# Performance work log

Hardware: AMD Instinct MI355X
Metric: run time of the kernel (lower is better)

## Reference

```python
import jax, jax.numpy as jnp
import numpy as np

B, N, D, K = 8, 4096, 128, 1024


def setup_inputs() -> dict:
    key = jax.random.key(0)
    kx, kp = jax.random.split(key)
    x = jax.random.normal(kx, (B, N, D), dtype=jnp.float32)
    # matches nn.Parameter(...).uniform_(-0.1, 0.1)
    prototypes = jax.random.uniform(kp, (K, D), dtype=jnp.float32, minval=-0.1, maxval=0.1)
    return {"x": x, "prototypes": prototypes, "hard": 1}


def reference(x, prototypes, hard):
    x_sq = jnp.sum(x * x, axis=-1, keepdims=True)            # [B,N,1]
    p_sq = jnp.sum(prototypes * prototypes, axis=-1)         # [K]
    xp = jnp.einsum('bnd,kd->bnk', x, prototypes)            # [B,N,K]
    scores = -(x_sq + p_sq[None, None, :] - 2.0 * xp)        # [B,N,K]
    if bool(hard):
        idx = jnp.argmax(scores, axis=-1)                    # [B,N]
        matched = prototypes[idx]                            # [B,N,D]
    else:
        w = jax.nn.softmax(scores, axis=-1)                  # [B,N,K]
        matched = jnp.einsum('bnk,kd->bnd', w, prototypes)   # [B,N,D]
    return (matched, scores)
```

## Files before the change

### kernel.cpp

```cpp
#include <hip/hip_runtime.h>

typedef short short8 __attribute__((ext_vector_type(8)));
typedef float f32x4  __attribute__((ext_vector_type(4)));

constexpr int M_TOT  = 8 * 4096;
constexpr int K_PROT = 1024;
constexpr int D_DIM  = 128;

constexpr size_t WS_PSQ_OFF = (size_t)M_TOT * 4;
constexpr size_t WS_PF_OFF  = WS_PSQ_OFF + (size_t)K_PROT * 4;

__device__ inline unsigned short bf16_hi(float f) {
  unsigned u = __builtin_bit_cast(unsigned, f);
  unsigned r = u + 0x7FFFu + ((u >> 16) & 1u);
  return (unsigned short)(r >> 16);
}
__device__ inline float bf16_tof(unsigned short h) {
  return __builtin_bit_cast(float, (unsigned)h << 16);
}

__device__ inline void barrier_lds() {
  asm volatile("s_waitcnt lgkmcnt(0)\n\ts_barrier" ::: "memory");
}

__global__ __launch_bounds__(256) void norms_kernel(
    const float* __restrict__ x, const float* __restrict__ p,
    float* __restrict__ xsq, float* __restrict__ psq) {
  int group = blockIdx.x * (blockDim.x >> 5) + (threadIdx.x >> 5);
  int lane  = threadIdx.x & 31;
  if (group >= M_TOT + K_PROT) return;
  const float* row = (group < M_TOT) ? (x + (size_t)group * D_DIM)
                                     : (p + (size_t)(group - M_TOT) * D_DIM);
  float4 v = reinterpret_cast<const float4*>(row)[lane];
  float s = v.x * v.x + v.y * v.y + v.z * v.z + v.w * v.w;
  #pragma unroll
  for (int off = 16; off > 0; off >>= 1) s += __shfl_down(s, off, 32);
  if (lane == 0) {
    if (group < M_TOT) xsq[group] = s;
    else psq[group - M_TOT] = s;
  }
}

__global__ __launch_bounds__(256) void pfrag_kernel(
    const float* __restrict__ p, short* __restrict__ pf) {
  int g    = blockIdx.x * 256 + threadIdx.x;
  int lane = g & 63;
  int s    = (g >> 6) & 7;
  int ng   = g >> 9;
  int part = s >> 2, ks = s & 3;
  int proto = ng * 16 + (lane & 15);
  int k0    = ks * 32 + (lane >> 4) * 8;
  const float4* pr = (const float4*)(p + (size_t)proto * D_DIM + k0);
  float4 a = pr[0], b = pr[1];
  float e[8] = {a.x, a.y, a.z, a.w, b.x, b.y, b.z, b.w};
  short8 frag;
  #pragma unroll
  for (int j = 0; j < 8; ++j) {
    unsigned short h = bf16_hi(e[j]);
    if (part) h = bf16_hi(e[j] - bf16_tof(h));
    frag[j] = (short)h;
  }
  *(short8*)(pf + (size_t)g * 8) = frag;
}

__global__ __launch_bounds__(256, 2) void proto_mfma(
    const float* __restrict__ x, const float* __restrict__ p,
    const short* __restrict__ pf, const float* __restrict__ xsq,
    const float* __restrict__ psq,
    float* __restrict__ matched, float* __restrict__ scores) {
  __shared__ short xlds[32 * 64 * 8];
  __shared__ float sbuf[64][132];
  __shared__ float sv[4][64];
  __shared__ int   si[4][64];
  __shared__ int   fidx[64];

  const int tid = threadIdx.x;
  const int w   = tid >> 6;
  const int l   = tid & 63;
  const int m0  = blockIdx.x * 64;

  #pragma unroll
  for (int i = 0; i < 8; ++i) {
    int piece = i * 256 + tid;
    int lane = piece & 63;
    int s = piece >> 6;
    int ks = s & 3, nt = (s >> 2) & 3, part = s >> 4;
    int pix = m0 + nt * 16 + (lane & 15);
    int k0  = ks * 32 + (lane >> 4) * 8;
    const float4* xr = (const float4*)(x + (size_t)pix * D_DIM + k0);
    float4 a = xr[0], b = xr[1];
    float e[8] = {a.x, a.y, a.z, a.w, b.x, b.y, b.z, b.w};
    short8 frag;
    #pragma unroll
    for (int j = 0; j < 8; ++j) {
      unsigned short h = bf16_hi(e[j]);
      if (part) h = bf16_hi(e[j] - bf16_tof(h));
      frag[j] = (short)h;
    }
    *(short8*)(xlds + (size_t)piece * 8) = frag;
  }
  __syncthreads();

  float xs[4];
  #pragma unroll
  for (int nt = 0; nt < 4; ++nt) xs[nt] = xsq[m0 + nt * 16 + (l & 15)];

  float best[4]; int bidx[4];
  #pragma unroll
  for (int nt = 0; nt < 4; ++nt) { best[nt] = -3.4e38f; bidx[nt] = 0; }

  for (int chunk = 0; chunk < 4; ++chunk) {
    f32x4 acc[4][4];
    #pragma unroll
    for (int mt = 0; mt < 4; ++mt)
      #pragma unroll
      for (int nt = 0; nt < 4; ++nt) acc[mt][nt] = (f32x4){0.f, 0.f, 0.f, 0.f};

    const int pgbase = chunk * 16 + w * 4;

    #pragma unroll
    for (int ks = 0; ks < 4; ++ks) {
      short8 pah[4], pal[4], bh[4], bl[4];
      #pragma unroll
      for (int mt = 0; mt < 4; ++mt) {
        pah[mt] = *(const short8*)(pf + ((size_t)((pgbase + mt) * 8 + ks) * 64 + l) * 8);
        pal[mt] = *(const short8*)(pf + ((size_t)((pgbase + mt) * 8 + 4 + ks) * 64 + l) * 8);
      }
      #pragma unroll
      for (int nt = 0; nt < 4; ++nt) {
        bh[nt] = *(const short8*)(xlds + (size_t)(((nt * 4 + ks) * 64) + l) * 8);
        bl[nt] = *(const short8*)(xlds + (size_t)(((16 + nt * 4 + ks) * 64) + l) * 8);
      }
      #pragma unroll
      for (int mt = 0; mt < 4; ++mt)
        #pragma unroll
        for (int nt = 0; nt < 4; ++nt)
          acc[mt][nt] = __builtin_amdgcn_mfma_f32_16x16x32_bf16(pah[mt], bh[nt], acc[mt][nt], 0, 0, 0);
      #pragma unroll
      for (int mt = 0; mt < 4; ++mt)
        #pragma unroll
        for (int nt = 0; nt < 4; ++nt)
          acc[mt][nt] = __builtin_amdgcn_mfma_f32_16x16x32_bf16(pah[mt], bl[nt], acc[mt][nt], 0, 0, 0);
      #pragma unroll
      for (int mt = 0; mt < 4; ++mt)
        #pragma unroll
        for (int nt = 0; nt < 4; ++nt)
          acc[mt][nt] = __builtin_amdgcn_mfma_f32_16x16x32_bf16(pal[mt], bh[nt], acc[mt][nt], 0, 0, 0);
    }

    #pragma unroll
    for (int mt = 0; mt < 4; ++mt) {
      int pbase = chunk * 256 + w * 64 + mt * 16 + (l >> 4) * 4;
      float psa[4];
      *(float4*)psa = *(const float4*)(psq + pbase);
      #pragma unroll
      for (int nt = 0; nt < 4; ++nt) {
        f32x4 o;
        {
          #pragma clang fp contract(off)
          #pragma unroll
          for (int r = 0; r < 4; ++r) {
            float t = (xs[nt] + psa[r]) - 2.0f * acc[mt][nt][r];
            o[r] = -t;
            if (o[r] > best[nt]) { best[nt] = o[r]; bidx[nt] = pbase + r; }
          }
        }
        acc[mt][nt] = o;
      }
    }

    #pragma unroll
    for (int h = 0; h < 2; ++h) {
      if ((w >> 1) == h) {
        const int colbase = (w & 1) * 64 + (l >> 4) * 4;
        #pragma unroll
        for (int mt = 0; mt < 4; ++mt)
          #pragma unroll
          for (int nt = 0; nt < 4; ++nt)
            *(f32x4*)&sbuf[nt * 16 + (l & 15)][colbase + mt * 16] = acc[mt][nt];
      }
      barrier_lds();
      const int gbase = chunk * 256 + h * 128;
      #pragma unroll
      for (int ps = 0; ps < 8; ++ps) {
        int idx = ps * 256 + tid;
        int row = idx >> 5;
        int f4  = idx & 31;
        f32x4 v = *(const f32x4*)&sbuf[row][f4 * 4];
        *((f32x4*)(scores + (size_t)(m0 + row) * K_PROT + gbase + f4 * 4)) = v;
      }
      barrier_lds();
    }
  }

  #pragma unroll
  for (int nt = 0; nt < 4; ++nt) {
    #pragma unroll
    for (int m = 16; m <= 32; m <<= 1) {
      float ov = __shfl_xor(best[nt], m);
      int   oi = __shfl_xor(bidx[nt], m);
      if (ov > best[nt] || (ov == best[nt] && oi < bidx[nt])) {
        best[nt] = ov; bidx[nt] = oi;
      }
    }
  }
  if (l < 16) {
    #pragma unroll
    for (int nt = 0; nt < 4; ++nt) {
      sv[w][nt * 16 + l] = best[nt];
      si[w][nt * 16 + l] = bidx[nt];
    }
  }
  __syncthreads();
  if (tid < 64) {
    float v = sv[0][tid]; int bi = si[0][tid];
    #pragma unroll
    for (int e = 1; e < 4; ++e) {
      float vv = sv[e][tid]; int ii = si[e][tid];
      if (vv > v || (vv == v && ii < bi)) { v = vv; bi = ii; }
    }
    fidx[tid] = bi;
  }
  __syncthreads();

  for (int q = tid; q < 64 * 32; q += 256) {
    int pix = q >> 5, f4 = q & 31;
    float4 v = ((const float4*)(p + (size_t)fidx[pix] * D_DIM))[f4];
    *((f32x4*)(matched + (size_t)(m0 + pix) * D_DIM) + f4) = *(f32x4*)&v;
  }
}

extern "C" void kernel_launch(void* const* d_in, const int* in_sizes, int n_in,
                              void* d_out, int out_size, void* d_ws, size_t ws_size,
                              hipStream_t stream) {
  const float* x = (const float*)d_in[0];
  const float* p = (const float*)d_in[1];

  float* matched = (float*)d_out;
  float* scores  = (float*)d_out + (size_t)M_TOT * D_DIM;

  float* xsq = (float*)d_ws;
  float* psq = (float*)((char*)d_ws + WS_PSQ_OFF);
  short* pf  = (short*)((char*)d_ws + WS_PF_OFF);

  {
    int rows = M_TOT + K_PROT;
    int blocks = (rows + 7) / 8;
    norms_kernel<<<blocks, 256, 0, stream>>>(x, p, xsq, psq);
  }
  pfrag_kernel<<<128, 256, 0, stream>>>(p, pf);
  proto_mfma<<<M_TOT / 64, 256, 0, stream>>>(x, p, pf, xsq, psq, matched, scores);
}
```

Baseline: 184.7 us.

## Use per-wave swizzled LDS score staging, prefetch next-chunk fragments, merge prep kernels

Replaces the block-wide shared score buffer, which needed two barriers per half-chunk, with a per-wave XOR-swizzled LDS tile, so each wave writes out its own scores without block barriers. Prefetches the first-k-slice prototype fragments and the psq values for the next chunk while the stores drain. Merges the norms and fragment-prep kernels into one launch. LDS use rises to 32KB for score staging, which may reduce occupancy, and the prefetch raises register pressure.

```diff
diff --git a/kernel.cpp b/kernel.cpp
--- a/kernel.cpp
+++ b/kernel.cpp
@@ -9,6 +9,9 @@
 
 constexpr size_t WS_PSQ_OFF = (size_t)M_TOT * 4;
 constexpr size_t WS_PF_OFF  = WS_PSQ_OFF + (size_t)K_PROT * 4;
+
+constexpr int NORM_BLOCKS  = (M_TOT + K_PROT) / 8;
+constexpr int PFRAG_BLOCKS = 32768 / 256;
 
 __device__ inline unsigned short bf16_hi(float f) {
   unsigned u = __builtin_bit_cast(unsigned, f);
@@ -19,48 +22,45 @@
   return __builtin_bit_cast(float, (unsigned)h << 16);
 }
 
-__device__ inline void barrier_lds() {
-  asm volatile("s_waitcnt lgkmcnt(0)\n\ts_barrier" ::: "memory");
-}
-
-__global__ __launch_bounds__(256) void norms_kernel(
+__global__ __launch_bounds__(256) void prep_kernel(
     const float* __restrict__ x, const float* __restrict__ p,
-    float* __restrict__ xsq, float* __restrict__ psq) {
-  int group = blockIdx.x * (blockDim.x >> 5) + (threadIdx.x >> 5);
-  int lane  = threadIdx.x & 31;
-  if (group >= M_TOT + K_PROT) return;
-  const float* row = (group < M_TOT) ? (x + (size_t)group * D_DIM)
-                                     : (p + (size_t)(group - M_TOT) * D_DIM);
-  float4 v = reinterpret_cast<const float4*>(row)[lane];
-  float s = v.x * v.x + v.y * v.y + v.z * v.z + v.w * v.w;
-  #pragma unroll
-  for (int off = 16; off > 0; off >>= 1) s += __shfl_down(s, off, 32);
-  if (lane == 0) {
-    if (group < M_TOT) xsq[group] = s;
-    else psq[group - M_TOT] = s;
-  }
-}
-
-__global__ __launch_bounds__(256) void pfrag_kernel(
-    const float* __restrict__ p, short* __restrict__ pf) {
-  int g    = blockIdx.x * 256 + threadIdx.x;
-  int lane = g & 63;
-  int s    = (g >> 6) & 7;
-  int ng   = g >> 9;
-  int part = s >> 2, ks = s & 3;
-  int proto = ng * 16 + (lane & 15);
-  int k0    = ks * 32 + (lane >> 4) * 8;
-  const float4* pr = (const float4*)(p + (size_t)proto * D_DIM + k0);
-  float4 a = pr[0], b = pr[1];
-  float e[8] = {a.x, a.y, a.z, a.w, b.x, b.y, b.z, b.w};
-  short8 frag;
-  #pragma unroll
-  for (int j = 0; j < 8; ++j) {
-    unsigned short h = bf16_hi(e[j]);
-    if (part) h = bf16_hi(e[j] - bf16_tof(h));
-    frag[j] = (short)h;
-  }
-  *(short8*)(pf + (size_t)g * 8) = frag;
+    float* __restrict__ xsq, float* __restrict__ psq, short* __restrict__ pf) {
+  const int bx  = blockIdx.x;
+  const int tid = threadIdx.x;
+  if (bx < NORM_BLOCKS) {
+    int group = bx * 8 + (tid >> 5);
+    int lane  = tid & 31;
+    if (group >= M_TOT + K_PROT) return;
+    const float* row = (group < M_TOT) ? (x + (size_t)group * D_DIM)
+                                       : (p + (size_t)(group - M_TOT) * D_DIM);
+    float4 v = reinterpret_cast<const float4*>(row)[lane];
+    float s = v.x * v.x + v.y * v.y + v.z * v.z + v.w * v.w;
+    #pragma unroll
+    for (int off = 16; off > 0; off >>= 1) s += __shfl_down(s, off, 32);
+    if (lane == 0) {
+      if (group < M_TOT) xsq[group] = s;
+      else psq[group - M_TOT] = s;
+    }
+  } else {
+    int g    = (bx - NORM_BLOCKS) * 256 + tid;
+    int lane = g & 63;
+    int s    = (g >> 6) & 7;
+    int ng   = g >> 9;
+    int part = s >> 2, ks = s & 3;
+    int proto = ng * 16 + (lane & 15);
+    int k0    = ks * 32 + (lane >> 4) * 8;
+    const float4* pr = (const float4*)(p + (size_t)proto * D_DIM + k0);
+    float4 a = pr[0], b = pr[1];
+    float e[8] = {a.x, a.y, a.z, a.w, b.x, b.y, b.z, b.w};
+    short8 frag;
+    #pragma unroll
+    for (int j = 0; j < 8; ++j) {
+      unsigned short h = bf16_hi(e[j]);
+      if (part) h = bf16_hi(e[j] - bf16_tof(h));
+      frag[j] = (short)h;
+    }
+    *(short8*)(pf + (size_t)g * 8) = frag;
+  }
 }
 
 __global__ __launch_bounds__(256, 2) void proto_mfma(
@@ -69,24 +69,24 @@
     const float* __restrict__ psq,
     float* __restrict__ matched, float* __restrict__ scores) {
   __shared__ short xlds[32 * 64 * 8];
-  __shared__ float sbuf[64][132];
-  __shared__ float sv[4][64];
-  __shared__ int   si[4][64];
+  __shared__ float sw[4][2048];
+  __shared__ float svv[4][64];
+  __shared__ int   sii[4][64];
   __shared__ int   fidx[64];
 
-  const int tid = threadIdx.x;
-  const int w   = tid >> 6;
-  const int l   = tid & 63;
-  const int m0  = blockIdx.x * 64;
+  const int tid  = threadIdx.x;
+  const int w    = tid >> 6;
+  const int l    = tid & 63;
+  const int m0   = blockIdx.x * 64;
+  const int csub = (l >> 4) << 2;
 
   #pragma unroll
   for (int i = 0; i < 8; ++i) {
     int piece = i * 256 + tid;
-    int lane = piece & 63;
     int s = piece >> 6;
     int ks = s & 3, nt = (s >> 2) & 3, part = s >> 4;
-    int pix = m0 + nt * 16 + (lane & 15);
-    int k0  = ks * 32 + (lane >> 4) * 8;
+    int pix = m0 + nt * 16 + (l & 15);
+    int k0  = ks * 32 + (l >> 4) * 8;
     const float4* xr = (const float4*)(x + (size_t)pix * D_DIM + k0);
     float4 a = xr[0], b = xr[1];
     float e[8] = {a.x, a.y, a.z, a.w, b.x, b.y, b.z, b.w};
@@ -109,6 +109,18 @@
   #pragma unroll
   for (int nt = 0; nt < 4; ++nt) { best[nt] = -3.4e38f; bidx[nt] = 0; }
 
+  short8 ppah[4], ppal[4];
+  f32x4  cpsq[4];
+  {
+    const int pg0 = w * 4;
+    #pragma unroll
+    for (int mt = 0; mt < 4; ++mt) {
+      ppah[mt] = *(const short8*)(pf + ((size_t)((pg0 + mt) * 8 + 0) * 64 + l) * 8);
+      ppal[mt] = *(const short8*)(pf + ((size_t)((pg0 + mt) * 8 + 4) * 64 + l) * 8);
+      cpsq[mt] = *(const f32x4*)(psq + w * 64 + mt * 16 + csub);
+    }
+  }
+
   for (int chunk = 0; chunk < 4; ++chunk) {
     f32x4 acc[4][4];
     #pragma unroll
@@ -121,10 +133,15 @@
     #pragma unroll
     for (int ks = 0; ks < 4; ++ks) {
       short8 pah[4], pal[4], bh[4], bl[4];
-      #pragma unroll
-      for (int mt = 0; mt < 4; ++mt) {
-        pah[mt] = *(const short8*)(pf + ((size_t)((pgbase + mt) * 8 + ks) * 64 + l) * 8);
-        pal[mt] = *(const short8*)(pf + ((size_t)((pgbase + mt) * 8 + 4 + ks) * 64 + l) * 8);
+      if (ks == 0) {
+        #pragma unroll
+        for (int mt = 0; mt < 4; ++mt) { pah[mt] = ppah[mt]; pal[mt] = ppal[mt]; }
+      } else {
+        #pragma unroll
+        for (int mt = 0; mt < 4; ++mt) {
+          pah[mt] = *(const short8*)(pf + ((size_t)((pgbase + mt) * 8 + ks) * 64 + l) * 8);
+          pal[mt] = *(const short8*)(pf + ((size_t)((pgbase + mt) * 8 + 4 + ks) * 64 + l) * 8);
+        }
       }
       #pragma unroll
       for (int nt = 0; nt < 4; ++nt) {
@@ -150,9 +167,8 @@
 
     #pragma unroll
     for (int mt = 0; mt < 4; ++mt) {
-      int pbase = chunk * 256 + w * 64 + mt * 16 + (l >> 4) * 4;
-      float psa[4];
-      *(float4*)psa = *(const float4*)(psq + pbase);
+      int pbase = chunk * 256 + w * 64 + mt * 16 + csub;
+      float psa[4] = {cpsq[mt][0], cpsq[mt][1], cpsq[mt][2], cpsq[mt][3]};
       #pragma unroll
       for (int nt = 0; nt < 4; ++nt) {
         f32x4 o;
@@ -169,27 +185,38 @@
       }
     }
 
-    #pragma unroll
-    for (int h = 0; h < 2; ++h) {
-      if ((w >> 1) == h) {
-        const int colbase = (w & 1) * 64 + (l >> 4) * 4;
-        #pragma unroll
-        for (int mt = 0; mt < 4; ++mt)
-          #pragma unroll
-          for (int nt = 0; nt < 4; ++nt)
-            *(f32x4*)&sbuf[nt * 16 + (l & 15)][colbase + mt * 16] = acc[mt][nt];
-      }
-      barrier_lds();
-      const int gbase = chunk * 256 + h * 128;
+    if (chunk < 3) {
+      const int npg = pgbase + 16;
+      #pragma unroll
+      for (int mt = 0; mt < 4; ++mt) {
+        ppah[mt] = *(const short8*)(pf + ((size_t)((npg + mt) * 8 + 0) * 64 + l) * 8);
+        ppal[mt] = *(const short8*)(pf + ((size_t)((npg + mt) * 8 + 4) * 64 + l) * 8);
+        cpsq[mt] = *(const f32x4*)(psq + (chunk + 1) * 256 + w * 64 + mt * 16 + csub);
+      }
+    }
+
+    #pragma unroll
+    for (int mp = 0; mp < 2; ++mp) {
+      #pragma unroll
+      for (int mt2 = 0; mt2 < 2; ++mt2) {
+        int mt = mp * 2 + mt2;
+        #pragma unroll
+        for (int nt = 0; nt < 4; ++nt) {
+          int row = nt * 16 + (l & 15);
+          int col = mt2 * 16 + csub;
+          int idx = (row << 5) + (col ^ ((row & 7) << 2));
+          *(f32x4*)&sw[w][idx] = acc[mt][nt];
+        }
+      }
+      const int drow = l >> 3;
+      const int dcol = (l & 7) << 2;
       #pragma unroll
       for (int ps = 0; ps < 8; ++ps) {
-        int idx = ps * 256 + tid;
-        int row = idx >> 5;
-        int f4  = idx & 31;
-        f32x4 v = *(const f32x4*)&sbuf[row][f4 * 4];
-        *((f32x4*)(scores + (size_t)(m0 + row) * K_PROT + gbase + f4 * 4)) = v;
-      }
-      barrier_lds();
+        int row = (ps << 3) + drow;
+        int idx = (row << 5) + (dcol ^ (drow << 2));
+        f32x4 v = *(const f32x4*)&sw[w][idx];
+        *((f32x4*)(scores + (size_t)(m0 + row) * K_PROT + chunk * 256 + (w << 6) + (mp << 5)) + (l & 7)) = v;
+      }
     }
   }
 
@@ -207,16 +234,16 @@
   if (l < 16) {
     #pragma unroll
     for (int nt = 0; nt < 4; ++nt) {
-      sv[w][nt * 16 + l] = best[nt];
-      si[w][nt * 16 + l] = bidx[nt];
+      svv[w][nt * 16 + l] = best[nt];
+      sii[w][nt * 16 + l] = bidx[nt];
     }
   }
   __syncthreads();
   if (tid < 64) {
-    float v = sv[0][tid]; int bi = si[0][tid];
+    float v = svv[0][tid]; int bi = sii[0][tid];
     #pragma unroll
     for (int e = 1; e < 4; ++e) {
-      float vv = sv[e][tid]; int ii = si[e][tid];
+      float vv = svv[e][tid]; int ii = sii[e][tid];
       if (vv > v || (vv == v && ii < bi)) { v = vv; bi = ii; }
     }
     fidx[tid] = bi;
@@ -243,11 +270,6 @@
   float* psq = (float*)((char*)d_ws + WS_PSQ_OFF);
   short* pf  = (short*)((char*)d_ws + WS_PF_OFF);
 
-  {
-    int rows = M_TOT + K_PROT;
-    int blocks = (rows + 7) / 8;
-    norms_kernel<<<blocks, 256, 0, stream>>>(x, p, xsq, psq);
-  }
-  pfrag_kernel<<<128, 256, 0, stream>>>(p, pf);
+  prep_kernel<<<NORM_BLOCKS + PFRAG_BLOCKS, 256, 0, stream>>>(x, p, xsq, psq, pf);
   proto_mfma<<<M_TOT / 64, 256, 0, stream>>>(x, p, pf, xsq, psq, matched, scores);
 }
```

Measured after the change: 228.0 us. 1.23x slower.

## Merge prep kernels and shrink score staging buffer to raise occupancy

Applied to the files above, without the earlier changes.

Folds the norms and prototype-fragment kernels into one launch, removing one kernel launch and its gap. In the main kernel, the score staging buffer is halved to 64x68 and drained one wave's 64 columns at a time in four rounds instead of two. This lowers LDS use so launch bounds can ask for three blocks per CU instead of two. The cost is more barriers per chunk and tighter register limits, which may cause spills in the MFMA accumulator loop.

```diff
diff --git a/kernel.cpp b/kernel.cpp
--- a/kernel.cpp
+++ b/kernel.cpp
@@ -9,6 +9,9 @@
 
 constexpr size_t WS_PSQ_OFF = (size_t)M_TOT * 4;
 constexpr size_t WS_PF_OFF  = WS_PSQ_OFF + (size_t)K_PROT * 4;
+
+constexpr int NORM_BLOCKS  = (M_TOT + K_PROT) / 8;
+constexpr int PFRAG_BLOCKS = 32768 / 256;
 
 __device__ inline unsigned short bf16_hi(float f) {
   unsigned u = __builtin_bit_cast(unsigned, f);
@@ -23,70 +26,71 @@
   asm volatile("s_waitcnt lgkmcnt(0)\n\ts_barrier" ::: "memory");
 }
 
-__global__ __launch_bounds__(256) void norms_kernel(
+__global__ __launch_bounds__(256) void prep_kernel(
     const float* __restrict__ x, const float* __restrict__ p,
-    float* __restrict__ xsq, float* __restrict__ psq) {
-  int group = blockIdx.x * (blockDim.x >> 5) + (threadIdx.x >> 5);
-  int lane  = threadIdx.x & 31;
-  if (group >= M_TOT + K_PROT) return;
-  const float* row = (group < M_TOT) ? (x + (size_t)group * D_DIM)
-                                     : (p + (size_t)(group - M_TOT) * D_DIM);
-  float4 v = reinterpret_cast<const float4*>(row)[lane];
-  float s = v.x * v.x + v.y * v.y + v.z * v.z + v.w * v.w;
-  #pragma unroll
-  for (int off = 16; off > 0; off >>= 1) s += __shfl_down(s, off, 32);
-  if (lane == 0) {
-    if (group < M_TOT) xsq[group] = s;
-    else psq[group - M_TOT] = s;
-  }
-}
-
-__global__ __launch_bounds__(256) void pfrag_kernel(
-    const float* __restrict__ p, short* __restrict__ pf) {
-  int g    = blockIdx.x * 256 + threadIdx.x;
-  int lane = g & 63;
-  int s    = (g >> 6) & 7;
-  int ng   = g >> 9;
-  int part = s >> 2, ks = s & 3;
-  int proto = ng * 16 + (lane & 15);
-  int k0    = ks * 32 + (lane >> 4) * 8;
-  const float4* pr = (const float4*)(p + (size_t)proto * D_DIM + k0);
-  float4 a = pr[0], b = pr[1];
-  float e[8] = {a.x, a.y, a.z, a.w, b.x, b.y, b.z, b.w};
-  short8 frag;
-  #pragma unroll
-  for (int j = 0; j < 8; ++j) {
-    unsigned short h = bf16_hi(e[j]);
-    if (part) h = bf16_hi(e[j] - bf16_tof(h));
-    frag[j] = (short)h;
-  }
-  *(short8*)(pf + (size_t)g * 8) = frag;
-}
-
-__global__ __launch_bounds__(256, 2) void proto_mfma(
+    float* __restrict__ xsq, float* __restrict__ psq, short* __restrict__ pf) {
+  const int bx  = blockIdx.x;
+  const int tid = threadIdx.x;
+  if (bx < NORM_BLOCKS) {
+    int group = bx * 8 + (tid >> 5);
+    int lane  = tid & 31;
+    if (group >= M_TOT + K_PROT) return;
+    const float* row = (group < M_TOT) ? (x + (size_t)group * D_DIM)
+                                       : (p + (size_t)(group - M_TOT) * D_DIM);
+    float4 v = reinterpret_cast<const float4*>(row)[lane];
+    float s = v.x * v.x + v.y * v.y + v.z * v.z + v.w * v.w;
+    #pragma unroll
+    for (int off = 16; off > 0; off >>= 1) s += __shfl_down(s, off, 32);
+    if (lane == 0) {
+      if (group < M_TOT) xsq[group] = s;
+      else psq[group - M_TOT] = s;
+    }
+  } else {
+    int g    = (bx - NORM_BLOCKS) * 256 + tid;
+    int lane = g & 63;
+    int s    = (g >> 6) & 7;
+    int ng   = g >> 9;
+    int part = s >> 2, ks = s & 3;
+    int proto = ng * 16 + (lane & 15);
+    int k0    = ks * 32 + (lane >> 4) * 8;
+    const float4* pr = (const float4*)(p + (size_t)proto * D_DIM + k0);
+    float4 a = pr[0], b = pr[1];
+    float e[8] = {a.x, a.y, a.z, a.w, b.x, b.y, b.z, b.w};
+    short8 frag;
+    #pragma unroll
+    for (int j = 0; j < 8; ++j) {
+      unsigned short h = bf16_hi(e[j]);
+      if (part) h = bf16_hi(e[j] - bf16_tof(h));
+      frag[j] = (short)h;
+    }
+    *(short8*)(pf + (size_t)g * 8) = frag;
+  }
+}
+
+__global__ __launch_bounds__(256, 3) void proto_mfma(
     const float* __restrict__ x, const float* __restrict__ p,
     const short* __restrict__ pf, const float* __restrict__ xsq,
     const float* __restrict__ psq,
     float* __restrict__ matched, float* __restrict__ scores) {
   __shared__ short xlds[32 * 64 * 8];
-  __shared__ float sbuf[64][132];
+  __shared__ float sbuf[64][68];
   __shared__ float sv[4][64];
   __shared__ int   si[4][64];
   __shared__ int   fidx[64];
 
-  const int tid = threadIdx.x;
-  const int w   = tid >> 6;
-  const int l   = tid & 63;
-  const int m0  = blockIdx.x * 64;
+  const int tid  = threadIdx.x;
+  const int w    = tid >> 6;
+  const int l    = tid & 63;
+  const int m0   = blockIdx.x * 64;
+  const int csub = (l >> 4) << 2;
 
   #pragma unroll
   for (int i = 0; i < 8; ++i) {
     int piece = i * 256 + tid;
-    int lane = piece & 63;
     int s = piece >> 6;
     int ks = s & 3, nt = (s >> 2) & 3, part = s >> 4;
-    int pix = m0 + nt * 16 + (lane & 15);
-    int k0  = ks * 32 + (lane >> 4) * 8;
+    int pix = m0 + nt * 16 + (l & 15);
+    int k0  = ks * 32 + (l >> 4) * 8;
     const float4* xr = (const float4*)(x + (size_t)pix * D_DIM + k0);
     float4 a = xr[0], b = xr[1];
     float e[8] = {a.x, a.y, a.z, a.w, b.x, b.y, b.z, b.w};
@@ -150,7 +154,7 @@
 
     #pragma unroll
     for (int mt = 0; mt < 4; ++mt) {
-      int pbase = chunk * 256 + w * 64 + mt * 16 + (l >> 4) * 4;
+      int pbase = chunk * 256 + w * 64 + mt * 16 + csub;
       float psa[4];
       *(float4*)psa = *(const float4*)(psq + pbase);
       #pragma unroll
@@ -170,24 +174,22 @@
     }
 
     #pragma unroll
-    for (int h = 0; h < 2; ++h) {
-      if ((w >> 1) == h) {
-        const int colbase = (w & 1) * 64 + (l >> 4) * 4;
+    for (int r = 0; r < 4; ++r) {
+      if (w == r) {
         #pragma unroll
         for (int mt = 0; mt < 4; ++mt)
           #pragma unroll
           for (int nt = 0; nt < 4; ++nt)
-            *(f32x4*)&sbuf[nt * 16 + (l & 15)][colbase + mt * 16] = acc[mt][nt];
+            *(f32x4*)&sbuf[nt * 16 + (l & 15)][mt * 16 + csub] = acc[mt][nt];
       }
       barrier_lds();
-      const int gbase = chunk * 256 + h * 128;
-      #pragma unroll
-      for (int ps = 0; ps < 8; ++ps) {
+      #pragma unroll
+      for (int ps = 0; ps < 4; ++ps) {
         int idx = ps * 256 + tid;
-        int row = idx >> 5;
-        int f4  = idx & 31;
-        f32x4 v = *(const f32x4*)&sbuf[row][f4 * 4];
-        *((f32x4*)(scores + (size_t)(m0 + row) * K_PROT + gbase + f4 * 4)) = v;
+        int row = idx >> 4;
+        int c4  = idx & 15;
+        f32x4 v = *(const f32x4*)&sbuf[row][c4 * 4];
+        *((f32x4*)(scores + (size_t)(m0 + row) * K_PROT + chunk * 256 + r * 64) + c4) = v;
       }
       barrier_lds();
     }
@@ -243,11 +245,6 @@
   float* psq = (float*)((char*)d_ws + WS_PSQ_OFF);
   short* pf  = (short*)((char*)d_ws + WS_PF_OFF);
 
-  {
-    int rows = M_TOT + K_PROT;
-    int blocks = (rows + 7) / 8;
-    norms_kernel<<<blocks, 256, 0, stream>>>(x, p, xsq, psq);
-  }
-  pfrag_kernel<<<128, 256, 0, stream>>>(p, pf);
+  prep_kernel<<<NORM_BLOCKS + PFRAG_BLOCKS, 256, 0, stream>>>(x, p, xsq, psq, pf);
   proto_mfma<<<M_TOT / 64, 256, 0, stream>>>(x, p, pf, xsq, psq, matched, scores);
 }
```

New measurement: 187.7 us. Within noise of the previous version (+1.6%).
